# Optimization experiments

Measured on AMD Instinct MI355X. Metric: run time of the kernel, lower is better.

The kernel has to match this reference:

```python
import jax, jax.numpy as jnp
import numpy as np

H = 32        # num query heads
KVH = 8       # num kv heads
D = 128       # head_dim
ROPE_BASE = 10000.0
NEG_INF = jnp.finfo(jnp.float32).min


def rope_interleaved(x):
    """Interleaved (GPT-NeoX-style pairs (x0,x1),(x2,x3),...) RoPE. x: [b,s,h,d]."""
    d = x.shape[-1]
    inv_freq = 1.0 / (ROPE_BASE ** (jnp.arange(0, d, 2, dtype=jnp.float32) / d))  # [d/2]
    pos = jnp.arange(x.shape[1], dtype=jnp.float32)
    ang = pos[:, None] * inv_freq[None, :]                    # [s, d/2]
    cos = jnp.cos(ang)[None, :, None, :]
    sin = jnp.sin(ang)[None, :, None, :]
    xp = x.reshape(*x.shape[:-1], d // 2, 2)
    x1, x2 = xp[..., 0], xp[..., 1]
    r1 = x1 * cos - x2 * sin
    r2 = x1 * sin + x2 * cos
    return jnp.stack([r1, r2], axis=-1).reshape(x.shape)


def setup_inputs() -> dict:
    key = jax.random.key(0)
    k1, k2, k3 = jax.random.split(key, 3)
    B, S, E = 2, 2048, 4096
    x = jax.random.normal(k1, (B, S, E), dtype=jnp.float32)
    wqkv = jax.random.normal(k2, (E + 2 * KVH * D, E), dtype=jnp.float32) * 0.02
    wo = jax.random.normal(k3, (E, E), dtype=jnp.float32) * 0.02
    return {"x": x, "wqkv": wqkv, "wo": wo}


def reference(x, wqkv, wo):
    b, s, e = x.shape
    q_per_kv = H // KVH
    # fused QKV projection (torch Linear layout: y = x @ W.T)
    qkv = jnp.einsum('bse,fe->bsf', x, wqkv)
    # rearrange 'b s (h gs d) -> b s h gs d', gs = q_per_kv + 2
    qkv = qkv.reshape(b, s, KVH, q_per_kv + 2, D)
    q = qkv[..., :q_per_kv, :].reshape(b, s, H, D)   # (h gs) -> H query heads
    k = qkv[..., -2, :]                              # [b,s,KVH,D]
    v = qkv[..., -1, :]
    # RoPE (rotary_emb_dim == head_dim, interleaved)
    q = rope_interleaved(q)
    k = rope_interleaved(k)
    # GQA: expand kv heads to match query heads
    k = jnp.repeat(k, q_per_kv, axis=2)              # [b,s,H,D]
    v = jnp.repeat(v, q_per_kv, axis=2)
    scale = D ** -0.5
    scores = jnp.einsum('bqhd,bkhd->bhqk', q, k) * scale
    causal = jnp.tril(jnp.ones((s, s), dtype=bool))
    scores = jnp.where(causal[None, None], scores, NEG_INF)
    attn = jax.nn.softmax(scores, axis=-1)
    ctx = jnp.einsum('bhqk,bkhd->bqhd', attn, v).reshape(b, s, H * D)
    return jnp.einsum('bsf,ef->bse', ctx, wo)
```

## Files before the change

### kernel.cpp

```cpp
#include <hip/hip_runtime.h>
#include <cstdint>

typedef __bf16 bf16;
typedef __bf16 bf16x8 __attribute__((ext_vector_type(8)));
typedef float  f32x4  __attribute__((ext_vector_type(4)));

#define AS1(p) ((__attribute__((address_space(1))) void*)(p))
#define AS3(p) ((__attribute__((address_space(3))) void*)(p))

__device__ __forceinline__ void gload16(const void* g, void* l) {
  __builtin_amdgcn_global_load_lds(AS1(g), AS3(l), 16, 0, 0);
}

constexpr int B_ = 2, S_ = 2048, E_ = 4096, H_ = 32, KVH_ = 8, D_ = 128;
constexpr int QPK_ = H_ / KVH_;
constexpr int F_ = E_ + 2 * KVH_ * D_;
constexpr int M_ = B_ * S_;

__global__ void f2bf_k(const float* __restrict__ in, bf16* __restrict__ out, int n8) {
  int i = blockIdx.x * 256 + threadIdx.x;
  if (i >= n8) return;
  const float4* p = (const float4*)(in + (size_t)i * 8);
  float4 a = p[0], b = p[1];
  bf16x8 o;
  o[0] = (bf16)a.x; o[1] = (bf16)a.y; o[2] = (bf16)a.z; o[3] = (bf16)a.w;
  o[4] = (bf16)b.x; o[5] = (bf16)b.y; o[6] = (bf16)b.z; o[7] = (bf16)b.w;
  *(bf16x8*)(out + (size_t)i * 8) = o;
}

__global__ void rope_table_k(float2* __restrict__ tab) {
  int i = blockIdx.x * 256 + threadIdx.x;
  int s = i >> 6, f = i & 63;
  float inv = powf(10000.0f, -2.0f * (float)f / 128.0f);
  float ang = (float)s * inv;
  tab[i] = make_float2(cosf(ang), sinf(ang));
}

template <typename OutT>
__global__ __launch_bounds__(512, 2)
void gemm256(const bf16* __restrict__ A, const bf16* __restrict__ B,
             OutT* __restrict__ C, int M, int N, int K) {
  __shared__ bf16 As[2][16384];
  __shared__ bf16 Bs[2][16384];
  const int tid = threadIdx.x;
  const int wid = tid >> 6, lane = tid & 63;
  const int l15 = lane & 15, g = lane >> 4;
  const int wr = wid >> 2, wc = wid & 3;
  const int bm = blockIdx.x, bn = blockIdx.y;
  const bf16* Ab = A + (size_t)bm * 256 * K;
  const bf16* Bb = B + (size_t)bn * 256 * K;
  const int nT = K >> 6;
  const int swz = (l15 & 7) << 4;

  f32x4 acc[8][4];
#pragma unroll
  for (int m = 0; m < 8; ++m)
#pragma unroll
    for (int n = 0; n < 4; ++n) acc[m][n] = (f32x4){0.f, 0.f, 0.f, 0.f};

  auto stg = [&](const bf16* src, bf16* dst, int t, int h) {
#pragma unroll
    for (int i = 0; i < 2; ++i) {
      int lb = h * 16384 + i * 8192 + wid * 1024 + lane * 16;
      int row = lb >> 7;
      int colb = (lb & 127) ^ ((row & 7) << 4);
      gload16(src + (size_t)row * K + t * 64 + (colb >> 1),
              dst + ((h * 16384 + i * 8192 + wid * 1024) >> 1));
    }
  };

  bf16x8 af[4][2];
  bf16x8 bfr[2][2][2];

  stg(Bb, Bs[0], 0, 0); stg(Bb, Bs[0], 0, 1);
  stg(Ab, As[0], 0, 0); stg(Ab, As[0], 0, 1);
  if (nT > 1) {
    stg(Bb, Bs[1], 1, 0); stg(Bb, Bs[1], 1, 1);
    asm volatile("s_waitcnt vmcnt(4)");
  } else {
    asm volatile("s_waitcnt vmcnt(0)");
  }
  __builtin_amdgcn_sched_barrier(0);
  __builtin_amdgcn_s_barrier();

  for (int t = 0; t < nT; ++t) {
    const int cur = t & 1;
#pragma unroll
    for (int m = 0; m < 4; ++m) {
      int arow = wr * 128 + m * 16 + l15;
#pragma unroll
      for (int ks = 0; ks < 2; ++ks)
        af[m][ks] = *(const bf16x8*)&As[cur][(arow << 6) + (((ks * 64 + g * 16) ^ swz) >> 1)];
    }
#pragma unroll
    for (int n = 0; n < 2; ++n) {
      int brow = wc * 64 + n * 16 + l15;
#pragma unroll
      for (int ks = 0; ks < 2; ++ks)
        bfr[0][n][ks] = *(const bf16x8*)&Bs[cur][(brow << 6) + (((ks * 64 + g * 16) ^ swz) >> 1)];
    }
    if (t + 1 < nT) stg(Ab, As[cur ^ 1], t + 1, 0);
    __builtin_amdgcn_s_barrier();
    asm volatile("s_waitcnt lgkmcnt(0)");
    __builtin_amdgcn_s_setprio(1);
#pragma unroll
    for (int ks = 0; ks < 2; ++ks)
#pragma unroll
      for (int m = 0; m < 4; ++m)
#pragma unroll
        for (int n = 0; n < 2; ++n)
          acc[m][n] = __builtin_amdgcn_mfma_f32_16x16x32_bf16(af[m][ks], bfr[0][n][ks], acc[m][n], 0, 0, 0);
    __builtin_amdgcn_s_setprio(0);
    __builtin_amdgcn_s_barrier();
#pragma unroll
    for (int n = 0; n < 2; ++n) {
      int brow = wc * 64 + 32 + n * 16 + l15;
#pragma unroll
      for (int ks = 0; ks < 2; ++ks)
        bfr[1][n][ks] = *(const bf16x8*)&Bs[cur][(brow << 6) + (((ks * 64 + g * 16) ^ swz) >> 1)];
    }
    if (t + 1 < nT) stg(Ab, As[cur ^ 1], t + 1, 1);
    __builtin_amdgcn_s_barrier();
    asm volatile("s_waitcnt lgkmcnt(0)");
    __builtin_amdgcn_s_setprio(1);
#pragma unroll
    for (int ks = 0; ks < 2; ++ks)
#pragma unroll
      for (int m = 0; m < 4; ++m)
#pragma unroll
        for (int n = 0; n < 2; ++n)
          acc[m][2 + n] = __builtin_amdgcn_mfma_f32_16x16x32_bf16(af[m][ks], bfr[1][n][ks], acc[m][2 + n], 0, 0, 0);
    __builtin_amdgcn_s_setprio(0);
    __builtin_amdgcn_s_barrier();
#pragma unroll
    for (int m = 0; m < 4; ++m) {
      int arow = wr * 128 + 64 + m * 16 + l15;
#pragma unroll
      for (int ks = 0; ks < 2; ++ks)
        af[m][ks] = *(const bf16x8*)&As[cur][(arow << 6) + (((ks * 64 + g * 16) ^ swz) >> 1)];
    }
    if (t + 2 < nT) stg(Bb, Bs[cur], t + 2, 0);
    __builtin_amdgcn_s_barrier();
    asm volatile("s_waitcnt lgkmcnt(0)");
    __builtin_amdgcn_s_setprio(1);
#pragma unroll
    for (int ks = 0; ks < 2; ++ks)
#pragma unroll
      for (int m = 0; m < 4; ++m)
#pragma unroll
        for (int n = 0; n < 2; ++n)
          acc[4 + m][n] = __builtin_amdgcn_mfma_f32_16x16x32_bf16(af[m][ks], bfr[0][n][ks], acc[4 + m][n], 0, 0, 0);
    __builtin_amdgcn_s_setprio(0);
    __builtin_amdgcn_s_barrier();
    if (t + 2 < nT) stg(Bb, Bs[cur], t + 2, 1);
    __builtin_amdgcn_s_setprio(1);
#pragma unroll
    for (int ks = 0; ks < 2; ++ks)
#pragma unroll
      for (int m = 0; m < 4; ++m)
#pragma unroll
        for (int n = 0; n < 2; ++n)
          acc[4 + m][2 + n] = __builtin_amdgcn_mfma_f32_16x16x32_bf16(af[m][ks], bfr[1][ks == 0 ? n : n][ks], acc[4 + m][2 + n], 0, 0, 0);
    __builtin_amdgcn_s_setprio(0);
    if (t + 2 < nT)      { asm volatile("s_waitcnt vmcnt(4)"); }
    else if (t + 1 < nT) { asm volatile("s_waitcnt vmcnt(0)"); }
    __builtin_amdgcn_sched_barrier(0);
    __builtin_amdgcn_s_barrier();
  }

#pragma unroll
  for (int mh = 0; mh < 2; ++mh)
#pragma unroll
    for (int m = 0; m < 4; ++m) {
      int row0 = bm * 256 + wr * 128 + mh * 64 + m * 16 + g * 4;
#pragma unroll
      for (int nh = 0; nh < 2; ++nh)
#pragma unroll
        for (int n = 0; n < 2; ++n) {
          int col = bn * 256 + wc * 64 + nh * 32 + n * 16 + l15;
          f32x4 v = acc[mh * 4 + m][nh * 2 + n];
#pragma unroll
          for (int r = 0; r < 4; ++r)
            C[(size_t)(row0 + r) * N + col] = (OutT)v[r];
        }
    }
}

__global__ void rope_q_k(const bf16* __restrict__ qkv, const float2* __restrict__ tab,
                         bf16* __restrict__ qout) {
  int idx = blockIdx.x * 256 + threadIdx.x;
  int c = idx & 15;
  int h = (idx >> 4) & 31;
  int s = (idx >> 9) & 2047;
  int b = idx >> 20;
  int d0 = c * 8;
  int kvh = h >> 2, j = h & 3;
  const bf16* src = qkv + (size_t)(b * 2048 + s) * F_ + kvh * (QPK_ + 2) * D_ + j * D_ + d0;
  bf16x8 v = *(const bf16x8*)src;
  const float2* tb = tab + s * 64 + (d0 >> 1);
  bf16x8 o;
#pragma unroll
  for (int p = 0; p < 4; ++p) {
    float x0 = (float)v[2 * p], x1 = (float)v[2 * p + 1];
    float2 cs = tb[p];
    o[2 * p]     = (bf16)(x0 * cs.x - x1 * cs.y);
    o[2 * p + 1] = (bf16)(x0 * cs.y + x1 * cs.x);
  }
  *(bf16x8*)(qout + (((size_t)b * 2048 + s) * 32 + h) * 128 + d0) = o;
}

__global__ void rope_k_k(const bf16* __restrict__ qkv, const float2* __restrict__ tab,
                         bf16* __restrict__ kout) {
  int idx = blockIdx.x * 256 + threadIdx.x;
  int c = idx & 15;
  int kvh = (idx >> 4) & 7;
  int s = (idx >> 7) & 2047;
  int b = idx >> 18;
  int d0 = c * 8;
  const bf16* src = qkv + (size_t)(b * 2048 + s) * F_ + kvh * (QPK_ + 2) * D_ + QPK_ * D_ + d0;
  bf16x8 v = *(const bf16x8*)src;
  const float2* tb = tab + s * 64 + (d0 >> 1);
  bf16x8 o;
#pragma unroll
  for (int p = 0; p < 4; ++p) {
    float x0 = (float)v[2 * p], x1 = (float)v[2 * p + 1];
    float2 cs = tb[p];
    o[2 * p]     = (bf16)(x0 * cs.x - x1 * cs.y);
    o[2 * p + 1] = (bf16)(x0 * cs.y + x1 * cs.x);
  }
  *(bf16x8*)(kout + ((size_t)(b * 8 + kvh) * 2048 + s) * 128 + d0) = o;
}

__global__ void vtrans_k(const bf16* __restrict__ qkv, bf16* __restrict__ vt) {
  int bidx = blockIdx.x;
  int st = bidx & 31;
  int dt = (bidx >> 5) & 3;
  int kvh = (bidx >> 7) & 7;
  int b = bidx >> 10;
  __shared__ bf16 tile[64][40];
  int t = threadIdx.x;
  {
    int sl = t >> 2, d0 = (t & 3) * 8;
    bf16x8 v = *(const bf16x8*)(qkv + (size_t)(b * 2048 + st * 64 + sl) * F_ +
                                kvh * (QPK_ + 2) * D_ + (QPK_ + 1) * D_ + dt * 32 + d0);
#pragma unroll
    for (int i = 0; i < 8; ++i) tile[sl][d0 + i] = v[i];
  }
  __syncthreads();
  {
    int dl = t >> 3, s0 = (t & 7) * 8;
    bf16x8 o;
#pragma unroll
    for (int i = 0; i < 8; ++i) o[i] = tile[s0 + i][dl];
    *(bf16x8*)(vt + ((size_t)(b * 8 + kvh) * 128 + dt * 32 + dl) * 2048 + st * 64 + s0) = o;
  }
}

__global__ __launch_bounds__(256, 2)
void attn_k(const bf16* __restrict__ q, const bf16* __restrict__ k,
            const bf16* __restrict__ vt, bf16* __restrict__ ctx) {
  int bid = blockIdx.x;
  int qp = bid & 15;
  int h = (bid >> 4) & 31;
  int b = bid >> 9;
  int kvh = h >> 2;
  int tid = threadIdx.x, w = tid >> 6, lane = tid & 63;
  int l15 = lane & 15, g = lane >> 4;

  __shared__ bf16 Ks[2][64 * 128];
  __shared__ bf16 Vs[2][128 * 64];
  __shared__ bf16 Plds[4][16 * 80];

  bf16* Pw = &Plds[w][0];
  const float C2 = 0.08838834764831845f * 1.4426950408889634f;
  const float NEG = -3.0e38f;

  const bf16* kb_base = k + (size_t)(b * 8 + kvh) * 2048 * 128;
  const bf16* vt_base = vt + (size_t)(b * 8 + kvh) * 128 * 2048;

  auto stage = [&](int kv0, int buf) {
#pragma unroll
    for (int i = 0; i < 4; ++i) {
      int lt = i * 4096 + tid * 16;
      int row = lt >> 8;
      int ch = (lt >> 4) & 15;
      int srcel = (ch ^ (row & 7)) << 3;
      gload16(kb_base + (size_t)(kv0 + row) * 128 + srcel,
              &Ks[buf][i * 2048 + w * 512]);
    }
#pragma unroll
    for (int i = 0; i < 4; ++i) {
      int lt = i * 4096 + tid * 16;
      int row = lt >> 7;
      int ch = (lt >> 4) & 7;
      int srcel = (ch ^ (row & 7)) << 3;
      gload16(vt_base + (size_t)row * 2048 + kv0 + srcel,
              &Vs[buf][i * 2048 + w * 512]);
    }
  };

  const int kxor = (l15 & 7) << 4;

  for (int pass = 0; pass < 2; ++pass) {
    int qt = pass ? (31 - qp) : qp;
    int qrow0 = qt * 64 + w * 16;

    bf16x8 aq[4];
#pragma unroll
    for (int ks = 0; ks < 4; ++ks)
      aq[ks] = *(const bf16x8*)(q + (((size_t)b * 2048 + qrow0 + l15) * 32 + h) * 128 + ks * 32 + g * 8);

    f32x4 acco[8];
#pragma unroll
    for (int n = 0; n < 8; ++n) acco[n] = (f32x4){0.f, 0.f, 0.f, 0.f};
    float m_r[4] = {NEG, NEG, NEG, NEG};
    float l_r[4] = {0.f, 0.f, 0.f, 0.f};

    int cur = 0;
    stage(0, 0);
    __syncthreads();

    const int nk = qt + 1;
    for (int kt = 0; kt < nk; ++kt) {
      int kv0 = kt * 64;
      if (kt + 1 < nk) stage(kv0 + 64, cur ^ 1);

      f32x4 s[4];
#pragma unroll
      for (int n = 0; n < 4; ++n) s[n] = (f32x4){0.f, 0.f, 0.f, 0.f};
#pragma unroll
      for (int ks = 0; ks < 4; ++ks) {
        int off = ((ks * 64 + g * 16) ^ kxor) >> 1;
#pragma unroll
        for (int n = 0; n < 4; ++n) {
          bf16x8 kb = *(const bf16x8*)&Ks[cur][(n * 16 + l15) * 128 + off];
          s[n] = __builtin_amdgcn_mfma_f32_16x16x32_bf16(aq[ks], kb, s[n], 0, 0, 0);
        }
      }
      if (kt == qt) {
#pragma unroll
        for (int n = 0; n < 4; ++n)
#pragma unroll
          for (int r = 0; r < 4; ++r) {
            int qg = qrow0 + g * 4 + r;
            int kg = kv0 + n * 16 + l15;
            if (kg > qg) s[n][r] = NEG;
          }
      }
      float fac[4];
#pragma unroll
      for (int r = 0; r < 4; ++r) {
        float mx = fmaxf(fmaxf(s[0][r], s[1][r]), fmaxf(s[2][r], s[3][r]));
#pragma unroll
        for (int off = 1; off < 16; off <<= 1) mx = fmaxf(mx, __shfl_xor(mx, off));
        float mn = fmaxf(m_r[r], mx);
        fac[r] = exp2f((m_r[r] - mn) * C2);
        m_r[r] = mn;
      }
      float psum[4] = {0.f, 0.f, 0.f, 0.f};
#pragma unroll
      for (int n = 0; n < 4; ++n)
#pragma unroll
        for (int r = 0; r < 4; ++r) {
          float p = exp2f((s[n][r] - m_r[r]) * C2);
          psum[r] += p;
          Pw[(g * 4 + r) * 80 + n * 16 + l15] = (bf16)p;
        }
#pragma unroll
      for (int r = 0; r < 4; ++r) {
        float ps = psum[r];
#pragma unroll
        for (int off = 1; off < 16; off <<= 1) ps += __shfl_xor(ps, off);
        l_r[r] = l_r[r] * fac[r] + ps;
      }
#pragma unroll
      for (int n = 0; n < 8; ++n)
#pragma unroll
        for (int r = 0; r < 4; ++r) acco[n][r] *= fac[r];
      asm volatile("s_waitcnt lgkmcnt(0)" ::: "memory");
#pragma unroll
      for (int ks = 0; ks < 2; ++ks) {
        bf16x8 pa = *(const bf16x8*)&Pw[l15 * 80 + ks * 32 + g * 8];
        int off = ((ks * 64 + g * 16) ^ kxor) >> 1;
#pragma unroll
        for (int n = 0; n < 8; ++n) {
          bf16x8 vb = *(const bf16x8*)&Vs[cur][(n * 16 + l15) * 64 + off];
          acco[n] = __builtin_amdgcn_mfma_f32_16x16x32_bf16(pa, vb, acco[n], 0, 0, 0);
        }
      }
      __syncthreads();
      cur ^= 1;
    }

#pragma unroll
    for (int r = 0; r < 4; ++r) {
      float inv = 1.0f / l_r[r];
      int qg = qrow0 + g * 4 + r;
#pragma unroll
      for (int n = 0; n < 8; ++n)
        ctx[(((size_t)b * 2048 + qg) * 32 + h) * 128 + n * 16 + l15] = (bf16)(acco[n][r] * inv);
    }
    __syncthreads();
  }
}

extern "C" void kernel_launch(void* const* d_in, const int* in_sizes, int n_in,
                              void* d_out, int out_size, void* d_ws, size_t ws_size,
                              hipStream_t stream) {
  const float* x = (const float*)d_in[0];
  const float* wqkv = (const float*)d_in[1];
  const float* wo = (const float*)d_in[2];
  float* out = (float*)d_out;
  char* ws = (char*)d_ws;

  bf16* xbf    = (bf16*)(ws + 0);
  bf16* wqkvbf = (bf16*)(ws + 33554432);
  bf16* qkvbf  = (bf16*)(ws + 83886080);
  bf16* qbuf   = (bf16*)(ws + 134217728);
  bf16* kbuf   = (bf16*)(ws + 167772160);
  bf16* vtbuf  = (bf16*)(ws + 176160768);
  float2* tab  = (float2*)(ws + 184549376);

  f2bf_k<<<8192, 256, 0, stream>>>(x, xbf, M_ * E_ / 8);
  f2bf_k<<<12288, 256, 0, stream>>>(wqkv, wqkvbf, F_ * E_ / 8);
  rope_table_k<<<512, 256, 0, stream>>>(tab);

  gemm256<bf16><<<dim3(M_ / 256, F_ / 256), 512, 0, stream>>>(xbf, wqkvbf, qkvbf, M_, F_, E_);

  rope_q_k<<<8192, 256, 0, stream>>>(qkvbf, tab, qbuf);
  rope_k_k<<<2048, 256, 0, stream>>>(qkvbf, tab, kbuf);
  vtrans_k<<<2048, 256, 0, stream>>>(qkvbf, vtbuf);

  bf16* wobf = qkvbf;
  f2bf_k<<<8192, 256, 0, stream>>>(wo, wobf, E_ * E_ / 8);

  bf16* ctx = xbf;
  attn_k<<<1024, 256, 0, stream>>>(qbuf, kbuf, vtbuf, ctx);

  gemm256<float><<<dim3(M_ / 256, E_ / 256), 512, 0, stream>>>(ctx, wobf, out, M_, E_, E_);
}
```

Baseline: 602.1 us.

## Widen attention blocks to 128 queries with triple-buffered KV and swizzle GEMM grid

The attention kernel now uses 512-thread blocks covering 128 query rows per pass, so each K/V tile staged in shared memory is reused by twice as many warps. K/V staging moves to a 3-deep ring with explicit vmcnt waits and raw barriers in place of __syncthreads, keeping two tiles in flight. Warps skip KV tiles that lie entirely above their causal diagonal. Block IDs are remapped in both attention and GEMM to group blocks that share data (XCD-style swizzle), aiming for better L2 locality. The larger shared memory footprint (3 K and 3 V buffers) may limit occupancy, and warp-level skips cause load imbalance inside a block.

```diff
diff --git a/kernel.cpp b/kernel.cpp
--- a/kernel.cpp
+++ b/kernel.cpp
@@ -46,11 +46,15 @@
   const int wid = tid >> 6, lane = tid & 63;
   const int l15 = lane & 15, g = lane >> 4;
   const int wr = wid >> 2, wc = wid & 3;
-  const int bm = blockIdx.x, bn = blockIdx.y;
+  const int gx = gridDim.x, gy = gridDim.y;
+  const int id = blockIdx.y * gx + blockIdx.x;
+  const int cpx = (gx * gy) >> 3;
+  const int swz = (id & 7) * cpx + (id >> 3);
+  const int bm = swz / gy, bn = swz % gy;
   const bf16* Ab = A + (size_t)bm * 256 * K;
   const bf16* Bb = B + (size_t)bn * 256 * K;
   const int nT = K >> 6;
-  const int swz = (l15 & 7) << 4;
+  const int swzr = (l15 & 7) << 4;
 
   f32x4 acc[8][4];
 #pragma unroll
@@ -90,14 +94,14 @@
       int arow = wr * 128 + m * 16 + l15;
 #pragma unroll
       for (int ks = 0; ks < 2; ++ks)
-        af[m][ks] = *(const bf16x8*)&As[cur][(arow << 6) + (((ks * 64 + g * 16) ^ swz) >> 1)];
+        af[m][ks] = *(const bf16x8*)&As[cur][(arow << 6) + (((ks * 64 + g * 16) ^ swzr) >> 1)];
     }
 #pragma unroll
     for (int n = 0; n < 2; ++n) {
       int brow = wc * 64 + n * 16 + l15;
 #pragma unroll
       for (int ks = 0; ks < 2; ++ks)
-        bfr[0][n][ks] = *(const bf16x8*)&Bs[cur][(brow << 6) + (((ks * 64 + g * 16) ^ swz) >> 1)];
+        bfr[0][n][ks] = *(const bf16x8*)&Bs[cur][(brow << 6) + (((ks * 64 + g * 16) ^ swzr) >> 1)];
     }
     if (t + 1 < nT) stg(Ab, As[cur ^ 1], t + 1, 0);
     __builtin_amdgcn_s_barrier();
@@ -117,7 +121,7 @@
       int brow = wc * 64 + 32 + n * 16 + l15;
 #pragma unroll
       for (int ks = 0; ks < 2; ++ks)
-        bfr[1][n][ks] = *(const bf16x8*)&Bs[cur][(brow << 6) + (((ks * 64 + g * 16) ^ swz) >> 1)];
+        bfr[1][n][ks] = *(const bf16x8*)&Bs[cur][(brow << 6) + (((ks * 64 + g * 16) ^ swzr) >> 1)];
     }
     if (t + 1 < nT) stg(Ab, As[cur ^ 1], t + 1, 1);
     __builtin_amdgcn_s_barrier();
@@ -137,7 +141,7 @@
       int arow = wr * 128 + 64 + m * 16 + l15;
 #pragma unroll
       for (int ks = 0; ks < 2; ++ks)
-        af[m][ks] = *(const bf16x8*)&As[cur][(arow << 6) + (((ks * 64 + g * 16) ^ swz) >> 1)];
+        af[m][ks] = *(const bf16x8*)&As[cur][(arow << 6) + (((ks * 64 + g * 16) ^ swzr) >> 1)];
     }
     if (t + 2 < nT) stg(Bb, Bs[cur], t + 2, 0);
     __builtin_amdgcn_s_barrier();
@@ -160,7 +164,7 @@
       for (int m = 0; m < 4; ++m)
 #pragma unroll
         for (int n = 0; n < 2; ++n)
-          acc[4 + m][2 + n] = __builtin_amdgcn_mfma_f32_16x16x32_bf16(af[m][ks], bfr[1][ks == 0 ? n : n][ks], acc[4 + m][2 + n], 0, 0, 0);
+          acc[4 + m][2 + n] = __builtin_amdgcn_mfma_f32_16x16x32_bf16(af[m][ks], bfr[1][n][ks], acc[4 + m][2 + n], 0, 0, 0);
     __builtin_amdgcn_s_setprio(0);
     if (t + 2 < nT)      { asm volatile("s_waitcnt vmcnt(4)"); }
     else if (t + 1 < nT) { asm volatile("s_waitcnt vmcnt(0)"); }
@@ -256,20 +260,21 @@
   }
 }
 
-__global__ __launch_bounds__(256, 2)
+__global__ __launch_bounds__(512, 2)
 void attn_k(const bf16* __restrict__ q, const bf16* __restrict__ k,
             const bf16* __restrict__ vt, bf16* __restrict__ ctx) {
   int bid = blockIdx.x;
-  int qp = bid & 15;
-  int h = (bid >> 4) & 31;
-  int b = bid >> 9;
+  bid = (bid & 7) * 64 + (bid >> 3);
+  int qp = bid & 7;
+  int h = (bid >> 3) & 31;
+  int b = bid >> 8;
   int kvh = h >> 2;
   int tid = threadIdx.x, w = tid >> 6, lane = tid & 63;
   int l15 = lane & 15, g = lane >> 4;
 
-  __shared__ bf16 Ks[2][64 * 128];
-  __shared__ bf16 Vs[2][128 * 64];
-  __shared__ bf16 Plds[4][16 * 80];
+  __shared__ bf16 Ks[3][64 * 128];
+  __shared__ bf16 Vs[3][128 * 64];
+  __shared__ bf16 Plds[8][16 * 80];
 
   bf16* Pw = &Plds[w][0];
   const float C2 = 0.08838834764831845f * 1.4426950408889634f;
@@ -280,30 +285,30 @@
 
   auto stage = [&](int kv0, int buf) {
 #pragma unroll
-    for (int i = 0; i < 4; ++i) {
-      int lt = i * 4096 + tid * 16;
+    for (int i = 0; i < 2; ++i) {
+      int lt = i * 8192 + tid * 16;
       int row = lt >> 8;
       int ch = (lt >> 4) & 15;
       int srcel = (ch ^ (row & 7)) << 3;
       gload16(kb_base + (size_t)(kv0 + row) * 128 + srcel,
-              &Ks[buf][i * 2048 + w * 512]);
-    }
-#pragma unroll
-    for (int i = 0; i < 4; ++i) {
-      int lt = i * 4096 + tid * 16;
+              &Ks[buf][(i * 8192 + w * 1024) >> 1]);
+    }
+#pragma unroll
+    for (int i = 0; i < 2; ++i) {
+      int lt = i * 8192 + tid * 16;
       int row = lt >> 7;
       int ch = (lt >> 4) & 7;
       int srcel = (ch ^ (row & 7)) << 3;
       gload16(vt_base + (size_t)row * 2048 + kv0 + srcel,
-              &Vs[buf][i * 2048 + w * 512]);
+              &Vs[buf][(i * 8192 + w * 1024) >> 1]);
     }
   };
 
   const int kxor = (l15 & 7) << 4;
 
   for (int pass = 0; pass < 2; ++pass) {
-    int qt = pass ? (31 - qp) : qp;
-    int qrow0 = qt * 64 + w * 16;
+    int qt = pass ? (15 - qp) : qp;
+    int qrow0 = qt * 128 + w * 16;
 
     bf16x8 aq[4];
 #pragma unroll
@@ -316,80 +321,92 @@
     float m_r[4] = {NEG, NEG, NEG, NEG};
     float l_r[4] = {0.f, 0.f, 0.f, 0.f};
 
-    int cur = 0;
+    const int nk = 2 * qt + 2;
     stage(0, 0);
-    __syncthreads();
-
-    const int nk = qt + 1;
+    stage(64, 1);
+    asm volatile("s_waitcnt vmcnt(4)");
+    __builtin_amdgcn_sched_barrier(0);
+    __builtin_amdgcn_s_barrier();
+
     for (int kt = 0; kt < nk; ++kt) {
       int kv0 = kt * 64;
-      if (kt + 1 < nk) stage(kv0 + 64, cur ^ 1);
-
-      f32x4 s[4];
-#pragma unroll
-      for (int n = 0; n < 4; ++n) s[n] = (f32x4){0.f, 0.f, 0.f, 0.f};
-#pragma unroll
-      for (int ks = 0; ks < 4; ++ks) {
-        int off = ((ks * 64 + g * 16) ^ kxor) >> 1;
-#pragma unroll
-        for (int n = 0; n < 4; ++n) {
-          bf16x8 kb = *(const bf16x8*)&Ks[cur][(n * 16 + l15) * 128 + off];
-          s[n] = __builtin_amdgcn_mfma_f32_16x16x32_bf16(aq[ks], kb, s[n], 0, 0, 0);
+      int cur = kt % 3;
+      if (kt + 2 < nk) stage(kv0 + 128, (kt + 2) % 3);
+
+      if (kv0 <= qrow0 + 15) {
+        f32x4 s[4];
+#pragma unroll
+        for (int n = 0; n < 4; ++n) s[n] = (f32x4){0.f, 0.f, 0.f, 0.f};
+#pragma unroll
+        for (int ks = 0; ks < 4; ++ks) {
+          int off = ((ks * 64 + g * 16) ^ kxor) >> 1;
+#pragma unroll
+          for (int n = 0; n < 4; ++n) {
+            bf16x8 kb = *(const bf16x8*)&Ks[cur][(n * 16 + l15) * 128 + off];
+            s[n] = __builtin_amdgcn_mfma_f32_16x16x32_bf16(aq[ks], kb, s[n], 0, 0, 0);
+          }
+        }
+        if (kv0 + 63 > qrow0) {
+#pragma unroll
+          for (int n = 0; n < 4; ++n)
+#pragma unroll
+            for (int r = 0; r < 4; ++r) {
+              int qg = qrow0 + g * 4 + r;
+              int kg = kv0 + n * 16 + l15;
+              if (kg > qg) s[n][r] = NEG;
+            }
+        }
+        float fac[4];
+#pragma unroll
+        for (int r = 0; r < 4; ++r) {
+          float mx = fmaxf(fmaxf(s[0][r], s[1][r]), fmaxf(s[2][r], s[3][r]));
+#pragma unroll
+          for (int off = 1; off < 16; off <<= 1) mx = fmaxf(mx, __shfl_xor(mx, off));
+          float mn = fmaxf(m_r[r], mx);
+          fac[r] = exp2f((m_r[r] - mn) * C2);
+          m_r[r] = mn;
+        }
+        float psum[4] = {0.f, 0.f, 0.f, 0.f};
+#pragma unroll
+        for (int n = 0; n < 4; ++n)
+#pragma unroll
+          for (int r = 0; r < 4; ++r) {
+            float p = exp2f((s[n][r] - m_r[r]) * C2);
+            psum[r] += p;
+            Pw[(g * 4 + r) * 80 + n * 16 + l15] = (bf16)p;
+          }
+#pragma unroll
+        for (int r = 0; r < 4; ++r) {
+          float ps = psum[r];
+#pragma unroll
+          for (int off = 1; off < 16; off <<= 1) ps += __shfl_xor(ps, off);
+          l_r[r] = l_r[r] * fac[r] + ps;
+        }
+#pragma unroll
+        for (int n = 0; n < 8; ++n)
+#pragma unroll
+          for (int r = 0; r < 4; ++r) acco[n][r] *= fac[r];
+        __builtin_amdgcn_sched_barrier(0);
+        asm volatile("s_waitcnt lgkmcnt(0)");
+        __builtin_amdgcn_sched_barrier(0);
+#pragma unroll
+        for (int ks = 0; ks < 2; ++ks) {
+          bf16x8 pa = *(const bf16x8*)&Pw[l15 * 80 + ks * 32 + g * 8];
+          int off = ((ks * 64 + g * 16) ^ kxor) >> 1;
+#pragma unroll
+          for (int n = 0; n < 8; ++n) {
+            bf16x8 vb = *(const bf16x8*)&Vs[cur][(n * 16 + l15) * 64 + off];
+            acco[n] = __builtin_amdgcn_mfma_f32_16x16x32_bf16(pa, vb, acco[n], 0, 0, 0);
+          }
         }
       }
-      if (kt == qt) {
-#pragma unroll
-        for (int n = 0; n < 4; ++n)
-#pragma unroll
-          for (int r = 0; r < 4; ++r) {
-            int qg = qrow0 + g * 4 + r;
-            int kg = kv0 + n * 16 + l15;
-            if (kg > qg) s[n][r] = NEG;
-          }
+
+      if (kt + 1 < nk) {
+        if (kt + 2 < nk) { asm volatile("s_waitcnt vmcnt(4)"); }
+        else             { asm volatile("s_waitcnt vmcnt(0)"); }
+        __builtin_amdgcn_sched_barrier(0);
       }
-      float fac[4];
-#pragma unroll
-      for (int r = 0; r < 4; ++r) {
-        float mx = fmaxf(fmaxf(s[0][r], s[1][r]), fmaxf(s[2][r], s[3][r]));
-#pragma unroll
-        for (int off = 1; off < 16; off <<= 1) mx = fmaxf(mx, __shfl_xor(mx, off));
-        float mn = fmaxf(m_r[r], mx);
-        fac[r] = exp2f((m_r[r] - mn) * C2);
-        m_r[r] = mn;
-      }
-      float psum[4] = {0.f, 0.f, 0.f, 0.f};
-#pragma unroll
-      for (int n = 0; n < 4; ++n)
-#pragma unroll
-        for (int r = 0; r < 4; ++r) {
-          float p = exp2f((s[n][r] - m_r[r]) * C2);
-          psum[r] += p;
-          Pw[(g * 4 + r) * 80 + n * 16 + l15] = (bf16)p;
-        }
-#pragma unroll
-      for (int r = 0; r < 4; ++r) {
-        float ps = psum[r];
-#pragma unroll
-        for (int off = 1; off < 16; off <<= 1) ps += __shfl_xor(ps, off);
-        l_r[r] = l_r[r] * fac[r] + ps;
-      }
-#pragma unroll
-      for (int n = 0; n < 8; ++n)
-#pragma unroll
-        for (int r = 0; r < 4; ++r) acco[n][r] *= fac[r];
-      asm volatile("s_waitcnt lgkmcnt(0)" ::: "memory");
-#pragma unroll
-      for (int ks = 0; ks < 2; ++ks) {
-        bf16x8 pa = *(const bf16x8*)&Pw[l15 * 80 + ks * 32 + g * 8];
-        int off = ((ks * 64 + g * 16) ^ kxor) >> 1;
-#pragma unroll
-        for (int n = 0; n < 8; ++n) {
-          bf16x8 vb = *(const bf16x8*)&Vs[cur][(n * 16 + l15) * 64 + off];
-          acco[n] = __builtin_amdgcn_mfma_f32_16x16x32_bf16(pa, vb, acco[n], 0, 0, 0);
-        }
-      }
-      __syncthreads();
-      cur ^= 1;
+      __builtin_amdgcn_s_barrier();
     }
 
 #pragma unroll
@@ -400,7 +417,6 @@
       for (int n = 0; n < 8; ++n)
         ctx[(((size_t)b * 2048 + qg) * 32 + h) * 128 + n * 16 + l15] = (bf16)(acco[n][r] * inv);
     }
-    __syncthreads();
   }
 }
 
@@ -435,7 +451,7 @@
   f2bf_k<<<8192, 256, 0, stream>>>(wo, wobf, E_ * E_ / 8);
 
   bf16* ctx = xbf;
-  attn_k<<<1024, 256, 0, stream>>>(qbuf, kbuf, vtbuf, ctx);
+  attn_k<<<512, 512, 0, stream>>>(qbuf, kbuf, vtbuf, ctx);
 
   gemm256<float><<<dim3(M_ / 256, E_ / 256), 512, 0, stream>>>(ctx, wobf, out, M_, E_, E_);
 }
```

After: 608.9 us. About the same (+1.1%).
